# Kernel tuning notes

Measured on AMD Instinct MI355X. Metric: run time of the kernel, lower is better.

## Reference

```python
import jax, jax.numpy as jnp
import numpy as np

INPUT_DIM = 66
OUTPUT_COUNT = 8192
NUM_PAIRS = 65536

def setup_inputs() -> dict:
    key = jax.random.key(0)
    k1, k2, k3, k4 = jax.random.split(key, 4)
    x = jax.random.normal(k1, (NUM_PAIRS, INPUT_DIM), dtype=jnp.float32)
    query = jax.random.normal(k2, (OUTPUT_COUNT, INPUT_DIM), dtype=jnp.float32)
    # nn.Linear(input_dim, input_dim): weight [out,in], bias [out]
    bound = 1.0 / np.sqrt(INPUT_DIM)
    Wk = jax.random.uniform(k3, (INPUT_DIM, INPUT_DIM), minval=-bound, maxval=bound, dtype=jnp.float32)
    bk = jax.random.uniform(k4, (INPUT_DIM,), minval=-bound, maxval=bound, dtype=jnp.float32)
    return {"x": x, "query": query, "Wk": Wk, "bk": bk}

def reference(x, query, Wk, bk):
    # K = Linear(x): x @ Wk^T + bk  -> [num_pairs, d]
    K = x @ Wk.T + bk
    # scores: [output_count, num_pairs]
    scores = jnp.einsum("qd,nd->qn", query, K)
    attn = jax.nn.softmax(scores, axis=1)
    # selected: [output_count, d] — note values are raw x, not K
    selected = attn @ x
    return selected
```

## Files before the change

### kernel.cpp

```cpp
#include <hip/hip_runtime.h>
#include <cstdint>


typedef __bf16    bf16x4 __attribute__((ext_vector_type(4)));
typedef __bf16    bf16x8 __attribute__((ext_vector_type(8)));
typedef _Float16  f16x4  __attribute__((ext_vector_type(4)));
typedef _Float16  f16x8  __attribute__((ext_vector_type(8)));
typedef float     f32x16 __attribute__((ext_vector_type(16)));

extern "C" __device__ float __ocml_native_exp2_f32(float);

#define NUM_PAIRS   65536
#define NUM_Q       8192
#define DIM         66
#define QPITCH      80
#define KFT         2560
#define XFT         3072
#define PARTP       68
#define NTILES      (NUM_PAIRS/32)

__device__ __forceinline__ f32x16 mfma_bf16(bf16x8 a, bf16x8 b, f32x16 c) {
    return __builtin_amdgcn_mfma_f32_32x32x16_bf16(a, b, c, 0, 0, 0);
}
__device__ __forceinline__ f32x16 mfma_f16(f16x8 a, f16x8 b, f32x16 c) {
    return __builtin_amdgcn_mfma_f32_32x32x16_f16(a, b, c, 0, 0, 0);
}
__device__ __forceinline__ void plswap(unsigned &a, unsigned &b) {
    asm("v_permlane32_swap_b32 %0, %1" : "+v"(a), "+v"(b));
}
__device__ __forceinline__ unsigned packbf(float a, float b) {
    union { __bf16 h[2]; unsigned u; } t;
    t.h[0] = (__bf16)a; t.h[1] = (__bf16)b;
    return t.u;
}
union U4 { unsigned u[4]; bf16x8 v; };

__device__ __forceinline__ void makefrags(const f32x16 &s, U4 *f) {
    float P[16];
    #pragma unroll
    for (int r = 0; r < 16; ++r) P[r] = __ocml_native_exp2_f32(s[r]);
    unsigned E0 = packbf(P[0],  P[1]),  E1 = packbf(P[2],  P[3]);
    unsigned F0 = packbf(P[4],  P[5]),  F1 = packbf(P[6],  P[7]);
    plswap(E0, F0); plswap(E1, F1);
    f[0].u[0] = E0; f[0].u[1] = E1; f[0].u[2] = F0; f[0].u[3] = F1;
    unsigned G0 = packbf(P[8],  P[9]),  G1 = packbf(P[10], P[11]);
    unsigned H0 = packbf(P[12], P[13]), H1 = packbf(P[14], P[15]);
    plswap(G0, H0); plswap(G1, H1);
    f[1].u[0] = G0; f[1].u[1] = G1; f[1].u[2] = H0; f[1].u[3] = H1;
}

__device__ __forceinline__ void compute_tile(const f16x8 (&kc)[5], const bf16x8 (&xa)[6],
                                             const f16x8 (&aQ)[2][5], f32x16 (&o)[2][3]) {
    f32x16 s0 = {}, s1 = {};
    #pragma unroll
    for (int kk = 0; kk < 5; ++kk) {
        s0 = mfma_f16(kc[kk], aQ[0][kk], s0);
        s1 = mfma_f16(kc[kk], aQ[1][kk], s1);
    }
    U4 f0[2], f1[2];
    makefrags(s0, f0);
    makefrags(s1, f1);
    #pragma unroll
    for (int par = 0; par < 2; ++par)
        #pragma unroll
        for (int dt = 0; dt < 3; ++dt) {
            o[0][dt] = mfma_bf16(f0[par].v, xa[par * 3 + dt], o[0][dt]);
            o[1][dt] = mfma_bf16(f1[par].v, xa[par * 3 + dt], o[1][dt]);
        }
}

#define PAP 104
#define WQP 67
__global__ __launch_bounds__(256) void prep_kernel(
    const float* __restrict__ x, const float* __restrict__ query,
    const float* __restrict__ Wk,
    unsigned short* __restrict__ Af_u, unsigned short* __restrict__ Xf_u,
    unsigned short* __restrict__ Qh_u) {
    const int tid = threadIdx.x;
    if (blockIdx.x >= 512) {
        __shared__ float sWq[DIM * WQP];
        __shared__ float sq[16 * WQP];
        _Float16* Qh = (_Float16*)Qh_u;
        const int q0 = (blockIdx.x - 512) * 16;
        for (int i = tid; i < DIM * DIM; i += 256)
            sWq[(i % DIM) * WQP + (i / DIM)] = Wk[i];
        for (int i = tid; i < 16 * DIM; i += 256)
            sq[(i / DIM) * WQP + (i % DIM)] = query[(long)(q0 + i / DIM) * DIM + (i % DIM)];
        __syncthreads();
        for (int slot = tid; slot < 16 * QPITCH; slot += 256) {
            int qi = slot / QPITCH, c = slot % QPITCH;
            float acc = 0.f;
            if (c < DIM) {
                const float* qr = &sq[qi * WQP];
                const float* wr = &sWq[c * WQP];
                #pragma unroll 6
                for (int d = 0; d < DIM; ++d) acc += qr[d] * wr[d];
                acc *= 1.4426950408889634f;
            }
            Qh[(long)(q0 + qi) * QPITCH + c] = (_Float16)acc;
        }
        return;
    }
    _Float16* Af = (_Float16*)Af_u;
    __bf16*   Xf = (__bf16*)Xf_u;
    __shared__ _Float16 sxh[128 * PAP];
    const long n0 = (long)blockIdx.x * 128;

    for (int i = tid; i < 128 * 96; i += 256) {
        int r = i / 96, c = i % 96;
        sxh[r * PAP + c] = (_Float16)((c < DIM) ? x[(n0 + r) * DIM + c] : 0.f);
    }
    __syncthreads();

    for (int i = 0; i < 5; ++i) {
        int slot = i * 256 + tid;
        int tt = slot / 320, rem = slot % 320;
        int kk = rem / 64, l = rem % 64;
        const _Float16* src = &sxh[(32 * tt + (l & 31)) * PAP + kk * 16 + (l >> 5) * 8];
        f16x4 lo = *(const f16x4*)src;
        f16x4 hi = *(const f16x4*)(src + 4);
        f16x8 v = __builtin_shufflevector(lo, hi, 0, 1, 2, 3, 4, 5, 6, 7);
        *(f16x8*)&Af[((long)blockIdx.x * 4 + tt) * KFT + kk * 512 + l * 8] = v;
    }
    for (int i = 0; i < 6; ++i) {
        int slot = i * 256 + tid;
        int tt = slot / 384, rem = slot % 384;
        int c = rem / 64, l = rem % 64;
        int dt = c % 3, par = c / 3;
        int d = 32 * dt + (l & 31);
        int p0 = 32 * tt + 16 * par + 8 * (l >> 5);
        bf16x8 v;
        #pragma unroll
        for (int j = 0; j < 8; ++j) {
            float vv = 0.f;
            if (d < DIM) vv = (float)sxh[(p0 + j) * PAP + d];
            else if (d == DIM) vv = 1.f;
            v[j] = (__bf16)vv;
        }
        *(bf16x8*)&Xf[((long)blockIdx.x * 4 + tt) * XFT + c * 512 + l * 8] = v;
    }
}

__global__ __launch_bounds__(256, 2) void flash_kernel(
    const unsigned short* __restrict__ Qh_u, const unsigned short* __restrict__ Af_u,
    const unsigned short* __restrict__ Xf_u, float* __restrict__ Part, int NS) {
    const _Float16* Qh = (const _Float16*)Qh_u;
    const _Float16* Af = (const _Float16*)Af_u;
    const __bf16*   Xf = (const __bf16*)Xf_u;

    const int tid = threadIdx.x;
    const int lane = tid & 63, wave = tid >> 6;
    const int l31 = lane & 31, h = lane >> 5;
    const int qb = blockIdx.x / NS, ns = blockIdx.x % NS;
    const int tiles = NTILES / NS;
    const int qbase = qb * 256 + wave * 64;

    const _Float16* kf = Af + (long)(ns * tiles) * KFT + lane * 8;
    const __bf16*   xf = Xf + (long)(ns * tiles) * XFT + lane * 8;

    f16x8 aQ[2][5];
    #pragma unroll
    for (int qt = 0; qt < 2; ++qt)
        #pragma unroll
        for (int kk = 0; kk < 5; ++kk)
            aQ[qt][kk] = *(const f16x8*)&Qh[(long)(qbase + qt * 32 + l31) * QPITCH + kk * 16 + h * 8];

    f32x16 o[2][3] = {};

    f16x8  kA[5], kB[5];
    bf16x8 xA[6], xB[6];
    #pragma unroll
    for (int kk = 0; kk < 5; ++kk) kA[kk] = *(const f16x8*)(kf + kk * 512);
    #pragma unroll
    for (int c = 0; c < 6; ++c)    xA[c]  = *(const bf16x8*)(xf + c * 512);

    for (int t = 0; t < tiles; t += 2) {
        {
            const _Float16* kp = kf + (long)(t + 1) * KFT;
            const __bf16*   xp = xf + (long)(t + 1) * XFT;
            #pragma unroll
            for (int kk = 0; kk < 5; ++kk) kB[kk] = *(const f16x8*)(kp + kk * 512);
            #pragma unroll
            for (int c = 0; c < 6; ++c)    xB[c]  = *(const bf16x8*)(xp + c * 512);
        }
        compute_tile(kA, xA, aQ, o);
        if (t + 2 < tiles) {
            const _Float16* kp = kf + (long)(t + 2) * KFT;
            const __bf16*   xp = xf + (long)(t + 2) * XFT;
            #pragma unroll
            for (int kk = 0; kk < 5; ++kk) kA[kk] = *(const f16x8*)(kp + kk * 512);
            #pragma unroll
            for (int c = 0; c < 6; ++c)    xA[c]  = *(const bf16x8*)(xp + c * 512);
        }
        compute_tile(kB, xB, aQ, o);
    }

    #pragma unroll
    for (int qt = 0; qt < 2; ++qt)
        #pragma unroll
        for (int dt = 0; dt < 3; ++dt)
            #pragma unroll
            for (int r = 0; r < 16; ++r) {
                int row = (r & 3) + 8 * (r >> 2) + 4 * h;
                int q = qbase + qt * 32 + row;
                int d = dt * 32 + l31;
                if (d < DIM + 1)
                    Part[((long)q * NS + ns) * PARTP + d] = o[qt][dt][r];
            }
}

__global__ __launch_bounds__(256) void combine_kernel(
    const float* __restrict__ Part, float* __restrict__ out, int NS) {
    int q = blockIdx.x * 2 + (threadIdx.x >> 7);
    int d = threadIdx.x & 127;
    if (d >= DIM) return;
    const float* base = Part + (long)q * NS * PARTP;
    float num = 0.f, den = 0.f;
    #pragma unroll 4
    for (int s = 0; s < NS; ++s) {
        num += base[s * PARTP + d];
        den += base[s * PARTP + DIM];
    }
    out[(long)q * DIM + d] = num / den;
}

extern "C" void kernel_launch(void* const* d_in, const int* in_sizes, int n_in,
                              void* d_out, int out_size, void* d_ws, size_t ws_size,
                              hipStream_t stream) {
    const float* x     = (const float*)d_in[0];
    const float* query = (const float*)d_in[1];
    const float* Wk    = (const float*)d_in[2];
    float* out = (float*)d_out;
    char* ws = (char*)d_ws;

    unsigned short* Qh = (unsigned short*)(ws + 0);
    unsigned short* Af = (unsigned short*)(ws + 1310720);
    unsigned short* Xf = (unsigned short*)(ws + 11796480);
    float* Part        = (float*)(ws + 24379392);

    const int NS = 16;

    prep_kernel<<<1024, 256, 0, stream>>>(x, query, Wk, Af, Xf, Qh);
    flash_kernel<<<(NUM_Q / 256) * NS, 256, 0, stream>>>(Qh, Af, Xf, Part, NS);
    combine_kernel<<<NUM_Q / 2, 256, 0, stream>>>(Part, out, NS);
}
```

Baseline: 279.8 us.

## Software-pipeline score MFMAs one tile ahead of exp and PV MFMAs

Restructures the main loop so the QK^T score MFMAs for the next tile are issued between the exp/pack of the current scores and the PV MFMAs. This interleaves exp2 VALU work with independent matrix ops to hide latency. X fragments now use a single register buffer reloaded after use, and K is prefetched two tiles ahead with clamped indices. The trade-off is more live accumulator registers for the carried scores, with fewer registers held for X, and the X load now has less time to complete before it is needed.

```diff
diff --git a/kernel.cpp b/kernel.cpp
--- a/kernel.cpp
+++ b/kernel.cpp
@@ -49,24 +49,52 @@
     f[1].u[0] = G0; f[1].u[1] = G1; f[1].u[2] = H0; f[1].u[3] = H1;
 }
 
-__device__ __forceinline__ void compute_tile(const f16x8 (&kc)[5], const bf16x8 (&xa)[6],
-                                             const f16x8 (&aQ)[2][5], f32x16 (&o)[2][3]) {
-    f32x16 s0 = {}, s1 = {};
-    #pragma unroll
-    for (int kk = 0; kk < 5; ++kk) {
-        s0 = mfma_f16(kc[kk], aQ[0][kk], s0);
-        s1 = mfma_f16(kc[kk], aQ[1][kk], s1);
-    }
-    U4 f0[2], f1[2];
+__device__ __forceinline__ void pipe_step(
+    int t, int tiles, const _Float16* __restrict__ kf, const __bf16* __restrict__ xf,
+    f16x8 (&kPre)[5], const f16x8 (&kNext)[5], bf16x8 (&xR)[6],
+    const f16x8 (&aQ)[2][5], f32x16 &s0, f32x16 &s1, f32x16 (&o)[2][3]) {
+
+    {
+        long tk = (t + 2 < tiles) ? (long)(t + 2) : (long)(tiles - 1);
+        const _Float16* kp = kf + tk * KFT;
+        #pragma unroll
+        for (int kk = 0; kk < 5; ++kk) kPre[kk] = *(const f16x8*)(kp + kk * 512);
+    }
+
+    U4 f0[2];
     makefrags(s0, f0);
+    {
+        f32x16 ns = {};
+        #pragma unroll
+        for (int kk = 0; kk < 5; ++kk) ns = mfma_f16(kNext[kk], aQ[0][kk], ns);
+        s0 = ns;
+    }
+    #pragma unroll
+    for (int par = 0; par < 2; ++par)
+        #pragma unroll
+        for (int dt = 0; dt < 3; ++dt)
+            o[0][dt] = mfma_bf16(f0[par].v, xR[par * 3 + dt], o[0][dt]);
+
+    U4 f1[2];
     makefrags(s1, f1);
+    {
+        f32x16 ns = {};
+        #pragma unroll
+        for (int kk = 0; kk < 5; ++kk) ns = mfma_f16(kNext[kk], aQ[1][kk], ns);
+        s1 = ns;
+    }
     #pragma unroll
     for (int par = 0; par < 2; ++par)
         #pragma unroll
-        for (int dt = 0; dt < 3; ++dt) {
-            o[0][dt] = mfma_bf16(f0[par].v, xa[par * 3 + dt], o[0][dt]);
-            o[1][dt] = mfma_bf16(f1[par].v, xa[par * 3 + dt], o[1][dt]);
-        }
+        for (int dt = 0; dt < 3; ++dt)
+            o[1][dt] = mfma_bf16(f1[par].v, xR[par * 3 + dt], o[1][dt]);
+
+    {
+        long tx = (t + 1 < tiles) ? (long)(t + 1) : (long)(tiles - 1);
+        const __bf16* xp = xf + tx * XFT;
+        #pragma unroll
+        for (int c = 0; c < 6; ++c) xR[c] = *(const bf16x8*)(xp + c * 512);
+    }
 }
 
 #define PAP 104
@@ -166,33 +194,29 @@
             aQ[qt][kk] = *(const f16x8*)&Qh[(long)(qbase + qt * 32 + l31) * QPITCH + kk * 16 + h * 8];
 
     f32x16 o[2][3] = {};
-
     f16x8  kA[5], kB[5];
-    bf16x8 xA[6], xB[6];
+    bf16x8 xR[6];
+    f32x16 s0, s1;
+
     #pragma unroll
     for (int kk = 0; kk < 5; ++kk) kA[kk] = *(const f16x8*)(kf + kk * 512);
     #pragma unroll
-    for (int c = 0; c < 6; ++c)    xA[c]  = *(const bf16x8*)(xf + c * 512);
+    for (int c = 0; c < 6; ++c)    xR[c]  = *(const bf16x8*)(xf + c * 512);
+    #pragma unroll
+    for (int kk = 0; kk < 5; ++kk) kB[kk] = *(const f16x8*)(kf + KFT + kk * 512);
+    {
+        f32x16 a = {}, b = {};
+        #pragma unroll
+        for (int kk = 0; kk < 5; ++kk) {
+            a = mfma_f16(kA[kk], aQ[0][kk], a);
+            b = mfma_f16(kA[kk], aQ[1][kk], b);
+        }
+        s0 = a; s1 = b;
+    }
 
     for (int t = 0; t < tiles; t += 2) {
-        {
-            const _Float16* kp = kf + (long)(t + 1) * KFT;
-            const __bf16*   xp = xf + (long)(t + 1) * XFT;
-            #pragma unroll
-            for (int kk = 0; kk < 5; ++kk) kB[kk] = *(const f16x8*)(kp + kk * 512);
-            #pragma unroll
-            for (int c = 0; c < 6; ++c)    xB[c]  = *(const bf16x8*)(xp + c * 512);
-        }
-        compute_tile(kA, xA, aQ, o);
-        if (t + 2 < tiles) {
-            const _Float16* kp = kf + (long)(t + 2) * KFT;
-            const __bf16*   xp = xf + (long)(t + 2) * XFT;
-            #pragma unroll
-            for (int kk = 0; kk < 5; ++kk) kA[kk] = *(const f16x8*)(kp + kk * 512);
-            #pragma unroll
-            for (int c = 0; c < 6; ++c)    xA[c]  = *(const bf16x8*)(xp + c * 512);
-        }
-        compute_tile(kB, xB, aQ, o);
+        pipe_step(t,     tiles, kf, xf, kA, kB, xR, aQ, s0, s1, o);
+        pipe_step(t + 1, tiles, kf, xf, kB, kA, xR, aQ, s0, s1, o);
     }
 
     #pragma unroll
```

Measured after the change: 275.6 us. Within noise of the previous version (-1.5%).
